# Optimization experiments

Measured on AMD Instinct MI355X. Metric: run time of the kernel, lower is better.

Reference implementation:

```python
import jax, jax.numpy as jnp
import numpy as np
from jax import lax

BN_EPS = 1e-5

def conv_bn_prelu(x, w, b, scale, bias, a):
    # Conv2d(k=3, pad=1, stride=1) in NCHW / OIHW layout
    y = lax.conv_general_dilated(x, w, window_strides=(1, 1), padding='SAME',
                                 dimension_numbers=('NCHW', 'OIHW', 'NCHW'))
    y = y + b[None, :, None, None]
    # BatchNorm2d, training-mode batch statistics over (B, H, W)
    mean = jnp.mean(y, axis=(0, 2, 3), keepdims=True)
    var = jnp.var(y, axis=(0, 2, 3), keepdims=True)
    y = (y - mean) * lax.rsqrt(var + BN_EPS)
    y = y * scale[None, :, None, None] + bias[None, :, None, None]
    # PReLU with single shared slope parameter
    return jnp.where(y >= 0, y, a * y)

def setup_inputs() -> dict:
    key = jax.random.key(0)
    ks = jax.random.split(key, 7)
    B, C, H, W = 4, 64, 64, 64
    x = jax.random.normal(ks[0], (B, C, H, W), dtype=jnp.float32)
    conv_w = jax.random.normal(ks[1], (C, C, 3, 3), dtype=jnp.float32) * 0.05
    conv_b = jax.random.normal(ks[2], (C,), dtype=jnp.float32) * 0.05
    bn_scale = jax.random.uniform(ks[3], (C,), dtype=jnp.float32, minval=0.5, maxval=1.5)
    bn_bias = jax.random.normal(ks[4], (C,), dtype=jnp.float32) * 0.05
    prelu_a = jnp.full((1,), 0.25, dtype=jnp.float32)
    gamma = jax.random.normal(ks[5], (1,), dtype=jnp.float32)
    return {'x': x, 'conv_w': conv_w, 'conv_b': conv_b, 'bn_scale': bn_scale,
            'bn_bias': bn_bias, 'prelu_a': prelu_a, 'gamma': gamma}

def reference(x, conv_w, conv_b, bn_scale, bn_bias, prelu_a, gamma):
    B, C, H, W = x.shape
    N = H * W
    feat = conv_bn_prelu(x, conv_w, conv_b, bn_scale, bn_bias, prelu_a)  # (B,C,H,W)
    f = feat.reshape(B, C, N)  # proj_query = f^T, proj_key = f, proj_value = f
    # energy[b,i,j] = sum_c f[b,c,i] * f[b,c,j]  -> (B, N, N)
    energy = jnp.einsum('bci,bcj->bij', f, f)
    # energy_new = rowmax - energy, softmax over last dim
    energy_new = jnp.max(energy, axis=-1, keepdims=True) - energy
    attn = jax.nn.softmax(energy_new, axis=-1)
    # out = bmm(proj_value, attention^T): out[b,c,i] = sum_j f[b,c,j] * attn[b,i,j]
    out = jnp.einsum('bcj,bij->bci', f, attn).reshape(B, C, H, W)
    return gamma * out + feat
```

## Files before the change

kernel.cpp:

```cpp
#include <hip/hip_runtime.h>

constexpr int kB = 4, kC = 64, kH = 64, kW = 64, kN = kH * kW;
constexpr float kEps = 1e-5f;
constexpr int SPLIT = 8;

typedef __attribute__((ext_vector_type(8))) short short8;
typedef __attribute__((ext_vector_type(4))) float f32x4;
typedef unsigned short u16;

__device__ inline unsigned pkbf(float a, float b) {
  unsigned ua = __float_as_uint(a), ub = __float_as_uint(b);
  ua += 0x7fff + ((ua >> 16) & 1);
  ub += 0x7fff + ((ub >> 16) & 1);
  return (ua >> 16) | (ub & 0xffff0000u);
}

__device__ inline float fexp2(float x) { return __builtin_amdgcn_exp2f(x); }

__global__ __launch_bounds__(256) void prep_w_kernel(const float* __restrict__ w,
                                                     u16* __restrict__ wA) {
  int idx = blockIdx.x * 256 + threadIdx.x;
  if (idx < 64 * 576) {
    int oc = idx / 576, r = idx - oc * 576;
    int khw = r >> 6, ic = r & 63;
    float v = w[(oc * 64 + ic) * 9 + khw];
    unsigned u = __float_as_uint(v);
    u += 0x7fff + ((u >> 16) & 1);
    wA[idx] = (u16)(u >> 16);
  }
}

__global__ __launch_bounds__(256) void conv_kernel(const float* __restrict__ x,
                                                   const u16* __restrict__ wA,
                                                   const float* __restrict__ bias,
                                                   float* __restrict__ y,
                                                   float* __restrict__ sums) {
  const int tid = threadIdx.x;
  const int lane = tid & 63;
  const int wv = tid >> 6;
  const int bx = blockIdx.x;
  const int b = bx >> 7;
  const int h = (bx & 127) >> 1;
  const int w0 = (bx & 1) * 32;
  const int lw = lane & 15, lg = lane >> 4;

  __shared__ __align__(16) u16 xt[3 * 40 * 64];

#pragma unroll
  for (int rep = 0; rep < 4; ++rep) {
    int idx = rep * 256 + tid;
    if (idx < 960) {
      int kh = idx / 320;
      int t = idx - kh * 320;
      int gw = t >> 5, icp = t & 31;
      int wb = w0 - 4 + gw * 4;
      int hh = h + kh - 1;
      float4 va = {0.f, 0.f, 0.f, 0.f}, vb = {0.f, 0.f, 0.f, 0.f};
      if (hh >= 0 && hh < 64 && wb >= 0 && wb < 64) {
        va = *(const float4*)&x[((b * 64 + icp * 2) * 64 + hh) * 64 + wb];
        vb = *(const float4*)&x[((b * 64 + icp * 2 + 1) * 64 + hh) * 64 + wb];
      }
      float av[4] = {va.x, va.y, va.z, va.w};
      float bv[4] = {vb.x, vb.y, vb.z, vb.w};
#pragma unroll
      for (int j = 0; j < 4; ++j) {
        int wc = gw * 4 + j;
        *(unsigned*)&xt[(kh * 40 + wc) * 64 + (((icp >> 2) ^ (wc & 7)) * 8 + (icp & 3) * 2)] =
            pkbf(av[j], bv[j]);
      }
    }
  }
  __syncthreads();

  const int oc0 = wv * 16;
  short8 af[18];
#pragma unroll
  for (int kc = 0; kc < 18; ++kc)
    af[kc] = *(const short8*)&wA[(oc0 + lw) * 576 + kc * 32 + lg * 8];

  f32x4 acc[2];
  acc[0] = (f32x4){0.f, 0.f, 0.f, 0.f};
  acc[1] = (f32x4){0.f, 0.f, 0.f, 0.f};
#pragma unroll
  for (int kc = 0; kc < 18; ++kc) {
    const int khw = kc >> 1;
    const int kh = khw / 3, kwv = khw % 3;
#pragma unroll
    for (int nt = 0; nt < 2; ++nt) {
      int wc = nt * 16 + lw + kwv + 3;
      short8 bf = *(const short8*)&xt[(kh * 40 + wc) * 64 + ((((kc & 1) * 4 + lg) ^ (wc & 7)) * 8)];
      acc[nt] = __builtin_amdgcn_mfma_f32_16x16x32_bf16(af[kc], bf, acc[nt], 0, 0, 0);
    }
  }
  float yv[2][4];
#pragma unroll
  for (int r = 0; r < 4; ++r) {
    float bv = bias[oc0 + lg * 4 + r];
    yv[0][r] = acc[0][r] + bv;
    yv[1][r] = acc[1][r] + bv;
  }
#pragma unroll
  for (int nt = 0; nt < 2; ++nt)
#pragma unroll
    for (int r = 0; r < 4; ++r)
      y[((b * 64 + oc0 + lg * 4 + r) * 64 + h) * 64 + w0 + nt * 16 + lw] = yv[nt][r];
  float sv[4], qv[4];
#pragma unroll
  for (int r = 0; r < 4; ++r) {
    sv[r] = yv[0][r] + yv[1][r];
    qv[r] = yv[0][r] * yv[0][r] + yv[1][r] * yv[1][r];
  }
#pragma unroll
  for (int m = 1; m < 16; m <<= 1)
#pragma unroll
    for (int r = 0; r < 4; ++r) {
      sv[r] += __shfl_xor(sv[r], m);
      qv[r] += __shfl_xor(qv[r], m);
    }
  if (lw == 0) {
    const int bin = bx & 7;
#pragma unroll
    for (int r = 0; r < 4; ++r) {
      int oc = oc0 + lg * 4 + r;
      atomicAdd(&sums[bin * 128 + oc], sv[r]);
      atomicAdd(&sums[bin * 128 + 64 + oc], qv[r]);
    }
  }
}

__global__ __launch_bounds__(256) void pack_kernel(const float* __restrict__ y,
                                                   const float* __restrict__ sums,
                                                   const float* __restrict__ scale,
                                                   const float* __restrict__ bias,
                                                   const float* __restrict__ pa,
                                                   float* __restrict__ feat,
                                                   u16* __restrict__ fbfA,
                                                   u16* __restrict__ fbfQ,
                                                   u16* __restrict__ fbfB) {
  __shared__ float ls[64 * 65];
  __shared__ float ABl[128];
  const int tid = threadIdx.x;
  const int b = blockIdx.x >> 6;
  const int n0 = (blockIdx.x & 63) << 6;
  if (tid < 64) {
    float s = 0.f, q = 0.f;
#pragma unroll
    for (int bin = 0; bin < 8; ++bin) {
      s += sums[bin * 128 + tid];
      q += sums[bin * 128 + 64 + tid];
    }
    float mean = s * (1.f / 16384.f);
    float var = q * (1.f / 16384.f) - mean * mean;
    float A = scale[tid] * rsqrtf(var + kEps);
    ABl[tid] = A;
    ABl[64 + tid] = bias[tid] - mean * A;
  }
  __syncthreads();
  {
    const int c = tid >> 2, nj = (tid & 3) << 4;
    const float A = ABl[c], Bc = ABl[64 + c], a = pa[0];
    const float* yp = y + ((b * kC + c) * kN) + n0 + nj;
    float f[16];
#pragma unroll
    for (int v = 0; v < 4; ++v) {
      float4 xv = *(const float4*)(yp + v * 4);
      float t;
      t = fmaf(A, xv.x, Bc); f[v * 4 + 0] = t >= 0.f ? t : a * t;
      t = fmaf(A, xv.y, Bc); f[v * 4 + 1] = t >= 0.f ? t : a * t;
      t = fmaf(A, xv.z, Bc); f[v * 4 + 2] = t >= 0.f ? t : a * t;
      t = fmaf(A, xv.w, Bc); f[v * 4 + 3] = t >= 0.f ? t : a * t;
    }
    float* fo = feat + ((b * kC + c) * kN) + n0 + nj;
#pragma unroll
    for (int v = 0; v < 4; ++v) {
      float4 fv = {f[v * 4 + 0], f[v * 4 + 1], f[v * 4 + 2], f[v * 4 + 3]};
      *(float4*)(fo + v * 4) = fv;
    }
#pragma unroll
    for (int v = 0; v < 16; ++v) ls[c * 65 + nj + v] = f[v];
  }
  __syncthreads();
  {
    int chunk = tid >> 5, pt = chunk >> 1, kc = chunk & 1;
    int lp2 = (tid & 31) * 2;
    size_t cidx = ((size_t)((b * 256 + (n0 >> 4) + pt) * 2 + kc)) * 512;
    u16* dstA = fbfA + cidx;
    u16* dstQ = fbfQ + cidx;
    const float cl = -1.4426950408889634f;
#pragma unroll
    for (int e = 0; e < 2; ++e) {
      int L = lp2 + e;
      int n = pt * 16 + (L & 15);
      int cb = kc * 32 + (L >> 4) * 8;
      float v[8];
#pragma unroll
      for (int r = 0; r < 8; ++r) v[r] = ls[(cb + r) * 65 + n];
      uint4 o = {pkbf(v[0], v[1]), pkbf(v[2], v[3]), pkbf(v[4], v[5]), pkbf(v[6], v[7])};
      *(uint4*)&dstA[L * 8] = o;
      uint4 oq = {pkbf(v[0] * cl, v[1] * cl), pkbf(v[2] * cl, v[3] * cl),
                  pkbf(v[4] * cl, v[5] * cl), pkbf(v[6] * cl, v[7] * cl)};
      *(uint4*)&dstQ[L * 8] = oq;
    }
  }
  {
    int chunk = tid >> 5, jt = chunk >> 2, ct = chunk & 3;
    int lp2 = (tid & 31) * 2;
    u16* dst = fbfB + ((size_t)((b * 128 + (n0 >> 5) + jt) * 4 + ct)) * 512;
#pragma unroll
    for (int e = 0; e < 2; ++e) {
      int L = lp2 + e;
      int c = ct * 16 + (L & 15);
      int nb = jt * 32 + (L >> 4) * 8;
      float v[8];
#pragma unroll
      for (int r = 0; r < 8; ++r) v[r] = ls[c * 65 + nb + r];
      uint4 o = {pkbf(v[0], v[1]), pkbf(v[2], v[3]), pkbf(v[4], v[5]), pkbf(v[6], v[7])};
      *(uint4*)&dst[L * 8] = o;
    }
  }
}

__global__ __launch_bounds__(256, 2) void attn_kernel(const u16* __restrict__ fbfA,
                                                      const u16* __restrict__ fbfQ,
                                                      const u16* __restrict__ fbfB,
                                                      float* __restrict__ Op,
                                                      float* __restrict__ lp) {
  const int tid = threadIdx.x;
  const int lane = tid & 63;
  const int w = tid >> 6;
  const int bx = blockIdx.x;
  const int s = bx & 7, itb = (bx >> 3) & 15, b = bx >> 7;
  const int c15 = lane & 15, g = lane >> 4;

  __shared__ __align__(16) u16 Ps[4][64 * 40];
  u16* ps = &Ps[w][0];
  const int pw_off = c15 * 40 + g * 4;
  const int pr_off = c15 * 40 + g * 8;

  const uint4* fAb = (const uint4*)fbfA + (size_t)b * 32768 + lane;
  const uint4* fQb = (const uint4*)fbfQ + (size_t)b * 32768 + lane;
  const uint4* fBb = (const uint4*)fbfB + (size_t)b * 32768 + lane;

  uint4 qf[4][2];
  const int ptq = itb * 16 + w * 4;
#pragma unroll
  for (int it = 0; it < 4; ++it)
#pragma unroll
    for (int kc = 0; kc < 2; ++kc)
      qf[it][kc] = fQb[(size_t)((ptq + it) * 2 + kc) * 64];

  const short8 ones = {0x3F80, 0x3F80, 0x3F80, 0x3F80, 0x3F80, 0x3F80, 0x3F80, 0x3F80};

  f32x4 oacc[4][4];
  f32x4 lacc[4];
#pragma unroll
  for (int it = 0; it < 4; ++it) {
    lacc[it] = (f32x4){0.f, 0.f, 0.f, 0.f};
#pragma unroll
    for (int ct = 0; ct < 4; ++ct) oacc[it][ct] = (f32x4){0.f, 0.f, 0.f, 0.f};
  }

  const uint4* pA = fAb + (size_t)(s * 64) * 64;
  const uint4* pV = fBb + (size_t)(s * 64) * 64;

  uint4 vp0, vp1, vp2, vp3;
  {
    uint4 a00 = pA[0], a01 = pA[64], a10 = pA[128], a11 = pA[192];
    vp0 = pV[0]; vp1 = pV[64]; vp2 = pV[128]; vp3 = pV[192];
    pA += 256; pV += 256;
    f32x4 sv[2][4];
#pragma unroll
    for (int it = 0; it < 4; ++it) {
      f32x4 z0 = (f32x4){0.f, 0.f, 0.f, 0.f};
      z0 = __builtin_amdgcn_mfma_f32_16x16x32_bf16(*(short8*)&a00, *(short8*)&qf[it][0], z0, 0, 0, 0);
      z0 = __builtin_amdgcn_mfma_f32_16x16x32_bf16(*(short8*)&a01, *(short8*)&qf[it][1], z0, 0, 0, 0);
      sv[0][it] = z0;
      f32x4 z1 = (f32x4){0.f, 0.f, 0.f, 0.f};
      z1 = __builtin_amdgcn_mfma_f32_16x16x32_bf16(*(short8*)&a10, *(short8*)&qf[it][0], z1, 0, 0, 0);
      z1 = __builtin_amdgcn_mfma_f32_16x16x32_bf16(*(short8*)&a11, *(short8*)&qf[it][1], z1, 0, 0, 0);
      sv[1][it] = z1;
    }
#pragma unroll
    for (int it = 0; it < 4; ++it)
#pragma unroll
      for (int jt2 = 0; jt2 < 2; ++jt2) {
        float p0 = fexp2(sv[jt2][it][0]);
        float p1 = fexp2(sv[jt2][it][1]);
        float p2 = fexp2(sv[jt2][it][2]);
        float p3 = fexp2(sv[jt2][it][3]);
        uint2 d;
        d.x = __builtin_amdgcn_perm(__float_as_uint(p1), __float_as_uint(p0), 0x07060302u);
        d.y = __builtin_amdgcn_perm(__float_as_uint(p3), __float_as_uint(p2), 0x07060302u);
        *(uint2*)&ps[pw_off + it * 640 + jt2 * 16] = d;
      }
  }

#pragma unroll 2
  for (int jt = 1; jt < 16; ++jt) {
    short8 pf[4];
#pragma unroll
    for (int it = 0; it < 4; ++it) pf[it] = *(const short8*)&ps[pr_off + it * 640];
    uint4 a00 = pA[0], a01 = pA[64], a10 = pA[128], a11 = pA[192];
    uint4 vc0 = pV[0], vc1 = pV[64], vc2 = pV[128], vc3 = pV[192];
    pA += 256; pV += 256;
#pragma unroll
    for (int it = 0; it < 4; ++it) {
      lacc[it] = __builtin_amdgcn_mfma_f32_16x16x32_bf16(pf[it], ones, lacc[it], 0, 0, 0);
      oacc[it][0] = __builtin_amdgcn_mfma_f32_16x16x32_bf16(pf[it], *(short8*)&vp0, oacc[it][0], 0, 0, 0);
      oacc[it][1] = __builtin_amdgcn_mfma_f32_16x16x32_bf16(pf[it], *(short8*)&vp1, oacc[it][1], 0, 0, 0);
      oacc[it][2] = __builtin_amdgcn_mfma_f32_16x16x32_bf16(pf[it], *(short8*)&vp2, oacc[it][2], 0, 0, 0);
      oacc[it][3] = __builtin_amdgcn_mfma_f32_16x16x32_bf16(pf[it], *(short8*)&vp3, oacc[it][3], 0, 0, 0);
    }
    f32x4 sv[2][4];
#pragma unroll
    for (int it = 0; it < 4; ++it) {
      f32x4 z0 = (f32x4){0.f, 0.f, 0.f, 0.f};
      z0 = __builtin_amdgcn_mfma_f32_16x16x32_bf16(*(short8*)&a00, *(short8*)&qf[it][0], z0, 0, 0, 0);
      z0 = __builtin_amdgcn_mfma_f32_16x16x32_bf16(*(short8*)&a01, *(short8*)&qf[it][1], z0, 0, 0, 0);
      sv[0][it] = z0;
      f32x4 z1 = (f32x4){0.f, 0.f, 0.f, 0.f};
      z1 = __builtin_amdgcn_mfma_f32_16x16x32_bf16(*(short8*)&a10, *(short8*)&qf[it][0], z1, 0, 0, 0);
      z1 = __builtin_amdgcn_mfma_f32_16x16x32_bf16(*(short8*)&a11, *(short8*)&qf[it][1], z1, 0, 0, 0);
      sv[1][it] = z1;
    }
#pragma unroll
    for (int it = 0; it < 4; ++it)
#pragma unroll
      for (int jt2 = 0; jt2 < 2; ++jt2) {
        float p0 = fexp2(sv[jt2][it][0]);
        float p1 = fexp2(sv[jt2][it][1]);
        float p2 = fexp2(sv[jt2][it][2]);
        float p3 = fexp2(sv[jt2][it][3]);
        uint2 d;
        d.x = __builtin_amdgcn_perm(__float_as_uint(p1), __float_as_uint(p0), 0x07060302u);
        d.y = __builtin_amdgcn_perm(__float_as_uint(p3), __float_as_uint(p2), 0x07060302u);
        *(uint2*)&ps[pw_off + it * 640 + jt2 * 16] = d;
      }
    vp0 = vc0; vp1 = vc1; vp2 = vc2; vp3 = vc3;
  }
  {
    short8 pf[4];
#pragma unroll
    for (int it = 0; it < 4; ++it) pf[it] = *(const short8*)&ps[pr_off + it * 640];
#pragma unroll
    for (int it = 0; it < 4; ++it) {
      lacc[it] = __builtin_amdgcn_mfma_f32_16x16x32_bf16(pf[it], ones, lacc[it], 0, 0, 0);
      oacc[it][0] = __builtin_amdgcn_mfma_f32_16x16x32_bf16(pf[it], *(short8*)&vp0, oacc[it][0], 0, 0, 0);
      oacc[it][1] = __builtin_amdgcn_mfma_f32_16x16x32_bf16(pf[it], *(short8*)&vp1, oacc[it][1], 0, 0, 0);
      oacc[it][2] = __builtin_amdgcn_mfma_f32_16x16x32_bf16(pf[it], *(short8*)&vp2, oacc[it][2], 0, 0, 0);
      oacc[it][3] = __builtin_amdgcn_mfma_f32_16x16x32_bf16(pf[it], *(short8*)&vp3, oacc[it][3], 0, 0, 0);
    }
  }

  float* Ow = Op + (size_t)(bx * 4 + w) * 4096;
#pragma unroll
  for (int it = 0; it < 4; ++it)
#pragma unroll
    for (int ct = 0; ct < 4; ++ct)
#pragma unroll
      for (int r = 0; r < 4; ++r)
        Ow[(it * 16 + g * 4 + r) * 64 + ct * 16 + c15] = oacc[it][ct][r];
  if (c15 == 0) {
    float* lw_ = lp + (size_t)(bx * 4 + w) * 64;
#pragma unroll
    for (int it = 0; it < 4; ++it)
#pragma unroll
      for (int r = 0; r < 4; ++r) lw_[it * 16 + g * 4 + r] = lacc[it][r];
  }
}

__global__ __launch_bounds__(256) void combine_kernel(const float* __restrict__ Op,
                                                      const float* __restrict__ lp,
                                                      const float* __restrict__ feat,
                                                      const float* __restrict__ gamma_p,
                                                      float* __restrict__ out) {
  const int tid = threadIdx.x;
  const int bx = blockIdx.x;
  const int b = bx >> 6, it64 = bx & 63;
  const int itb = it64 >> 2, w = it64 & 3;
  __shared__ float tr[64 * 65];
  __shared__ float linv[64];
  if (tid < 64) {
    float sum = 0.f;
#pragma unroll
    for (int s = 0; s < SPLIT; ++s)
      sum += lp[(size_t)(((b * 16 + itb) * 8 + s) * 4 + w) * 64 + tid];
    linv[tid] = 1.f / sum;
  }
  __syncthreads();
  const float gm = gamma_p[0];
#pragma unroll
  for (int rr = 0; rr < 4; ++rr) {
    int flat4 = rr * 256 + tid;
    int i = flat4 >> 4, c4 = (flat4 & 15) * 4;
    float4 acc = {0.f, 0.f, 0.f, 0.f};
#pragma unroll
    for (int s = 0; s < SPLIT; ++s) {
      float4 v = *(const float4*)&Op[(size_t)(((b * 16 + itb) * 8 + s) * 4 + w) * 4096 + i * 64 + c4];
      acc.x += v.x; acc.y += v.y; acc.z += v.z; acc.w += v.w;
    }
    float sc = gm * linv[i];
    tr[(c4 + 0) * 65 + i] = acc.x * sc;
    tr[(c4 + 1) * 65 + i] = acc.y * sc;
    tr[(c4 + 2) * 65 + i] = acc.z * sc;
    tr[(c4 + 3) * 65 + i] = acc.w * sc;
  }
  __syncthreads();
#pragma unroll
  for (int rr = 0; rr < 4; ++rr) {
    int flat4 = rr * 256 + tid;
    int c = flat4 >> 4, i4 = (flat4 & 15) * 4;
    float4 fv = *(const float4*)&feat[(size_t)(b * 64 + c) * 4096 + it64 * 64 + i4];
    float4 ov;
    ov.x = tr[c * 65 + i4 + 0] + fv.x;
    ov.y = tr[c * 65 + i4 + 1] + fv.y;
    ov.z = tr[c * 65 + i4 + 2] + fv.z;
    ov.w = tr[c * 65 + i4 + 3] + fv.w;
    *(float4*)&out[(size_t)(b * 64 + c) * 4096 + it64 * 64 + i4] = ov;
  }
}

extern "C" void kernel_launch(void* const* d_in, const int* in_sizes, int n_in,
                              void* d_out, int out_size, void* d_ws, size_t ws_size,
                              hipStream_t stream) {
  (void)in_sizes; (void)n_in; (void)out_size; (void)ws_size;
  const float* x        = (const float*)d_in[0];
  const float* conv_w   = (const float*)d_in[1];
  const float* conv_b   = (const float*)d_in[2];
  const float* bn_scale = (const float*)d_in[3];
  const float* bn_bias  = (const float*)d_in[4];
  const float* prelu_a  = (const float*)d_in[5];
  const float* gamma    = (const float*)d_in[6];
  float* out = (float*)d_out;

  float* feat = (float*)d_ws;
  u16* fbfA = (u16*)(feat + kB * kC * kN);
  u16* fbfQ = fbfA + kB * kC * kN;
  u16* fbfB = fbfQ + kB * kC * kN;
  u16* wA = fbfB + kB * kC * kN;
  float* sums = (float*)(wA + 36864);
  float* Op = sums + 1024;
  float* lp = Op + (size_t)2048 * 4096;

  float* y = out;

  (void)hipMemsetAsync(sums, 0, 1024 * sizeof(float), stream);
  prep_w_kernel<<<144, 256, 0, stream>>>(conv_w, wA);
  conv_kernel<<<kB * kH * 2, 256, 0, stream>>>(x, wA, conv_b, y, sums);
  pack_kernel<<<kB * (kN / 64), 256, 0, stream>>>(y, sums, bn_scale, bn_bias, prelu_a,
                                                  feat, fbfA, fbfQ, fbfB);
  attn_kernel<<<kB * 16 * SPLIT, 256, 0, stream>>>(fbfA, fbfQ, fbfB, Op, lp);
  combine_kernel<<<kB * 64, 256, 0, stream>>>(Op, lp, feat, gamma, out);
}
```

Measured before the change: 124.5 us.

## Prefetch key tiles one step ahead and compute softmax row sums with shuffles

```diff
diff --git a/kernel.cpp b/kernel.cpp
--- a/kernel.cpp
+++ b/kernel.cpp
@@ -249,94 +249,121 @@
     for (int kc = 0; kc < 2; ++kc)
       qf[it][kc] = fQb[(size_t)((ptq + it) * 2 + kc) * 64];
 
-  const short8 ones = {0x3F80, 0x3F80, 0x3F80, 0x3F80, 0x3F80, 0x3F80, 0x3F80, 0x3F80};
-
   f32x4 oacc[4][4];
-  f32x4 lacc[4];
-#pragma unroll
-  for (int it = 0; it < 4; ++it) {
-    lacc[it] = (f32x4){0.f, 0.f, 0.f, 0.f};
+  float lacc[4] = {0.f, 0.f, 0.f, 0.f};
+#pragma unroll
+  for (int it = 0; it < 4; ++it)
 #pragma unroll
     for (int ct = 0; ct < 4; ++ct) oacc[it][ct] = (f32x4){0.f, 0.f, 0.f, 0.f};
-  }
 
   const uint4* pA = fAb + (size_t)(s * 64) * 64;
   const uint4* pV = fBb + (size_t)(s * 64) * 64;
 
-  uint4 vp0, vp1, vp2, vp3;
+  uint4 aN[4], vP[4], vC[4];
+
   {
-    uint4 a00 = pA[0], a01 = pA[64], a10 = pA[128], a11 = pA[192];
-    vp0 = pV[0]; vp1 = pV[64]; vp2 = pV[128]; vp3 = pV[192];
+    uint4 aC[4];
+#pragma unroll
+    for (int q = 0; q < 4; ++q) aC[q] = pA[q * 64];
+#pragma unroll
+    for (int q = 0; q < 4; ++q) vP[q] = pV[q * 64];
     pA += 256; pV += 256;
+#pragma unroll
+    for (int q = 0; q < 4; ++q) aN[q] = pA[q * 64];
+    pA += 256;
+
     f32x4 sv[2][4];
 #pragma unroll
     for (int it = 0; it < 4; ++it) {
       f32x4 z0 = (f32x4){0.f, 0.f, 0.f, 0.f};
-      z0 = __builtin_amdgcn_mfma_f32_16x16x32_bf16(*(short8*)&a00, *(short8*)&qf[it][0], z0, 0, 0, 0);
-      z0 = __builtin_amdgcn_mfma_f32_16x16x32_bf16(*(short8*)&a01, *(short8*)&qf[it][1], z0, 0, 0, 0);
+      z0 = __builtin_amdgcn_mfma_f32_16x16x32_bf16(*(short8*)&aC[0], *(short8*)&qf[it][0], z0, 0, 0, 0);
+      z0 = __builtin_amdgcn_mfma_f32_16x16x32_bf16(*(short8*)&aC[1], *(short8*)&qf[it][1], z0, 0, 0, 0);
       sv[0][it] = z0;
       f32x4 z1 = (f32x4){0.f, 0.f, 0.f, 0.f};
-      z1 = __builtin_amdgcn_mfma_f32_16x16x32_bf16(*(short8*)&a10, *(short8*)&qf[it][0], z1, 0, 0, 0);
-      z1 = __builtin_amdgcn_mfma_f32_16x16x32_bf16(*(short8*)&a11, *(short8*)&qf[it][1], z1, 0, 0, 0);
+      z1 = __builtin_amdgcn_mfma_f32_16x16x32_bf16(*(short8*)&aC[2], *(short8*)&qf[it][0], z1, 0, 0, 0);
+      z1 = __builtin_amdgcn_mfma_f32_16x16x32_bf16(*(short8*)&aC[3], *(short8*)&qf[it][1], z1, 0, 0, 0);
       sv[1][it] = z1;
     }
 #pragma unroll
-    for (int it = 0; it < 4; ++it)
+    for (int it = 0; it < 4; ++it) {
+      float p[8];
 #pragma unroll
       for (int jt2 = 0; jt2 < 2; ++jt2) {
-        float p0 = fexp2(sv[jt2][it][0]);
-        float p1 = fexp2(sv[jt2][it][1]);
-        float p2 = fexp2(sv[jt2][it][2]);
-        float p3 = fexp2(sv[jt2][it][3]);
+        p[jt2 * 4 + 0] = fexp2(sv[jt2][it][0]);
+        p[jt2 * 4 + 1] = fexp2(sv[jt2][it][1]);
+        p[jt2 * 4 + 2] = fexp2(sv[jt2][it][2]);
+        p[jt2 * 4 + 3] = fexp2(sv[jt2][it][3]);
         uint2 d;
-        d.x = __builtin_amdgcn_perm(__float_as_uint(p1), __float_as_uint(p0), 0x07060302u);
-        d.y = __builtin_amdgcn_perm(__float_as_uint(p3), __float_as_uint(p2), 0x07060302u);
+        d.x = pkbf(p[jt2 * 4 + 0], p[jt2 * 4 + 1]);
+        d.y = pkbf(p[jt2 * 4 + 2], p[jt2 * 4 + 3]);
         *(uint2*)&ps[pw_off + it * 640 + jt2 * 16] = d;
       }
-  }
-
-#pragma unroll 2
-  for (int jt = 1; jt < 16; ++jt) {
+      float rs = ((p[0] + p[1]) + (p[2] + p[3])) + ((p[4] + p[5]) + (p[6] + p[7]));
+      rs += __shfl_xor(rs, 16);
+      rs += __shfl_xor(rs, 32);
+      lacc[it] += rs;
+    }
+  }
+
+#pragma unroll
+  for (int n = 1; n < 16; ++n) {
+    uint4 aF[4];
+    if (n < 15) {
+#pragma unroll
+      for (int q = 0; q < 4; ++q) aF[q] = pA[q * 64];
+      pA += 256;
+    }
+#pragma unroll
+    for (int q = 0; q < 4; ++q) vC[q] = pV[q * 64];
+    pV += 256;
+
     short8 pf[4];
 #pragma unroll
     for (int it = 0; it < 4; ++it) pf[it] = *(const short8*)&ps[pr_off + it * 640];
-    uint4 a00 = pA[0], a01 = pA[64], a10 = pA[128], a11 = pA[192];
-    uint4 vc0 = pV[0], vc1 = pV[64], vc2 = pV[128], vc3 = pV[192];
-    pA += 256; pV += 256;
-#pragma unroll
-    for (int it = 0; it < 4; ++it) {
-      lacc[it] = __builtin_amdgcn_mfma_f32_16x16x32_bf16(pf[it], ones, lacc[it], 0, 0, 0);
-      oacc[it][0] = __builtin_amdgcn_mfma_f32_16x16x32_bf16(pf[it], *(short8*)&vp0, oacc[it][0], 0, 0, 0);
-      oacc[it][1] = __builtin_amdgcn_mfma_f32_16x16x32_bf16(pf[it], *(short8*)&vp1, oacc[it][1], 0, 0, 0);
-      oacc[it][2] = __builtin_amdgcn_mfma_f32_16x16x32_bf16(pf[it], *(short8*)&vp2, oacc[it][2], 0, 0, 0);
-      oacc[it][3] = __builtin_amdgcn_mfma_f32_16x16x32_bf16(pf[it], *(short8*)&vp3, oacc[it][3], 0, 0, 0);
+#pragma unroll
+    for (int it = 0; it < 4; ++it) {
+      oacc[it][0] = __builtin_amdgcn_mfma_f32_16x16x32_bf16(pf[it], *(short8*)&vP[0], oacc[it][0], 0, 0, 0);
+      oacc[it][1] = __builtin_amdgcn_mfma_f32_16x16x32_bf16(pf[it], *(short8*)&vP[1], oacc[it][1], 0, 0, 0);
+      oacc[it][2] = __builtin_amdgcn_mfma_f32_16x16x32_bf16(pf[it], *(short8*)&vP[2], oacc[it][2], 0, 0, 0);
+      oacc[it][3] = __builtin_amdgcn_mfma_f32_16x16x32_bf16(pf[it], *(short8*)&vP[3], oacc[it][3], 0, 0, 0);
     }
     f32x4 sv[2][4];
 #pragma unroll
     for (int it = 0; it < 4; ++it) {
       f32x4 z0 = (f32x4){0.f, 0.f, 0.f, 0.f};
-      z0 = __builtin_amdgcn_mfma_f32_16x16x32_bf16(*(short8*)&a00, *(short8*)&qf[it][0], z0, 0, 0, 0);
-      z0 = __builtin_amdgcn_mfma_f32_16x16x32_bf16(*(short8*)&a01, *(short8*)&qf[it][1], z0, 0, 0, 0);
+      z0 = __builtin_amdgcn_mfma_f32_16x16x32_bf16(*(short8*)&aN[0], *(short8*)&qf[it][0], z0, 0, 0, 0);
+      z0 = __builtin_amdgcn_mfma_f32_16x16x32_bf16(*(short8*)&aN[1], *(short8*)&qf[it][1], z0, 0, 0, 0);
       sv[0][it] = z0;
       f32x4 z1 = (f32x4){0.f, 0.f, 0.f, 0.f};
-      z1 = __builtin_amdgcn_mfma_f32_16x16x32_bf16(*(short8*)&a10, *(short8*)&qf[it][0], z1, 0, 0, 0);
-      z1 = __builtin_amdgcn_mfma_f32_16x16x32_bf16(*(short8*)&a11, *(short8*)&qf[it][1], z1, 0, 0, 0);
+      z1 = __builtin_amdgcn_mfma_f32_16x16x32_bf16(*(short8*)&aN[2], *(short8*)&qf[it][0], z1, 0, 0, 0);
+      z1 = __builtin_amdgcn_mfma_f32_16x16x32_bf16(*(short8*)&aN[3], *(short8*)&qf[it][1], z1, 0, 0, 0);
       sv[1][it] = z1;
     }
 #pragma unroll
-    for (int it = 0; it < 4; ++it)
+    for (int it = 0; it < 4; ++it) {
+      float p[8];
 #pragma unroll
       for (int jt2 = 0; jt2 < 2; ++jt2) {
-        float p0 = fexp2(sv[jt2][it][0]);
-        float p1 = fexp2(sv[jt2][it][1]);
-        float p2 = fexp2(sv[jt2][it][2]);
-        float p3 = fexp2(sv[jt2][it][3]);
+        p[jt2 * 4 + 0] = fexp2(sv[jt2][it][0]);
+        p[jt2 * 4 + 1] = fexp2(sv[jt2][it][1]);
+        p[jt2 * 4 + 2] = fexp2(sv[jt2][it][2]);
+        p[jt2 * 4 + 3] = fexp2(sv[jt2][it][3]);
         uint2 d;
-        d.x = __builtin_amdgcn_perm(__float_as_uint(p1), __float_as_uint(p0), 0x07060302u);
-        d.y = __builtin_amdgcn_perm(__float_as_uint(p3), __float_as_uint(p2), 0x07060302u);
+        d.x = pkbf(p[jt2 * 4 + 0], p[jt2 * 4 + 1]);
+        d.y = pkbf(p[jt2 * 4 + 2], p[jt2 * 4 + 3]);
         *(uint2*)&ps[pw_off + it * 640 + jt2 * 16] = d;
       }
-    vp0 = vc0; vp1 = vc1; vp2 = vc2; vp3 = vc3;
+      float rs = ((p[0] + p[1]) + (p[2] + p[3])) + ((p[4] + p[5]) + (p[6] + p[7]));
+      rs += __shfl_xor(rs, 16);
+      rs += __shfl_xor(rs, 32);
+      lacc[it] += rs;
+    }
+#pragma unroll
+    for (int q = 0; q < 4; ++q) { vP[q] = vC[q]; }
+    if (n < 15) {
+#pragma unroll
+      for (int q = 0; q < 4; ++q) aN[q] = aF[q];
+    }
   }
   {
     short8 pf[4];
@@ -344,11 +371,10 @@
     for (int it = 0; it < 4; ++it) pf[it] = *(const short8*)&ps[pr_off + it * 640];
 #pragma unroll
     for (int it = 0; it < 4; ++it) {
-      lacc[it] = __builtin_amdgcn_mfma_f32_16x16x32_bf16(pf[it], ones, lacc[it], 0, 0, 0);
-      oacc[it][0] = __builtin_amdgcn_mfma_f32_16x16x32_bf16(pf[it], *(short8*)&vp0, oacc[it][0], 0, 0, 0);
-      oacc[it][1] = __builtin_amdgcn_mfma_f32_16x16x32_bf16(pf[it], *(short8*)&vp1, oacc[it][1], 0, 0, 0);
-      oacc[it][2] = __builtin_amdgcn_mfma_f32_16x16x32_bf16(pf[it], *(short8*)&vp2, oacc[it][2], 0, 0, 0);
-      oacc[it][3] = __builtin_amdgcn_mfma_f32_16x16x32_bf16(pf[it], *(short8*)&vp3, oacc[it][3], 0, 0, 0);
+      oacc[it][0] = __builtin_amdgcn_mfma_f32_16x16x32_bf16(pf[it], *(short8*)&vP[0], oacc[it][0], 0, 0, 0);
+      oacc[it][1] = __builtin_amdgcn_mfma_f32_16x16x32_bf16(pf[it], *(short8*)&vP[1], oacc[it][1], 0, 0, 0);
+      oacc[it][2] = __builtin_amdgcn_mfma_f32_16x16x32_bf16(pf[it], *(short8*)&vP[2], oacc[it][2], 0, 0, 0);
+      oacc[it][3] = __builtin_amdgcn_mfma_f32_16x16x32_bf16(pf[it], *(short8*)&vP[3], oacc[it][3], 0, 0, 0);
     }
   }
 
@@ -360,12 +386,10 @@
 #pragma unroll
       for (int r = 0; r < 4; ++r)
         Ow[(it * 16 + g * 4 + r) * 64 + ct * 16 + c15] = oacc[it][ct][r];
-  if (c15 == 0) {
+  if (lane < 16) {
     float* lw_ = lp + (size_t)(bx * 4 + w) * 64;
 #pragma unroll
-    for (int it = 0; it < 4; ++it)
-#pragma unroll
-      for (int r = 0; r < 4; ++r) lw_[it * 16 + g * 4 + r] = lacc[it][r];
+    for (int it = 0; it < 4; ++it) lw_[it * 16 + lane] = lacc[it];
   }
 }
 
```

Result: slower. 142.9 us (+14.7%).
